# Performance work log

Measured on AMD Instinct MI355X. Metric: run time of the kernel, lower is better.

Reference implementation:

```python
import jax, jax.numpy as jnp
import numpy as np

DIM = 4096
N_HEADS = 32
N_KV = 8
HEAD_DIM = 128
WINDOW = 4096
BSZ = 1
SEQ = 2048
REPEATS = N_HEADS // N_KV
SCALE = HEAD_DIM ** -0.5
NEG_INF = -1e9


def setup_inputs() -> dict:
    key = jax.random.key(0)
    ks = jax.random.split(key, 5)
    x = jax.random.normal(ks[0], (1, BSZ, SEQ, DIM), jnp.float32)
    wq = jax.random.normal(ks[1], (N_HEADS * HEAD_DIM, DIM), jnp.float32) * (DIM ** -0.5)
    wk = jax.random.normal(ks[2], (N_KV * HEAD_DIM, DIM), jnp.float32) * (DIM ** -0.5)
    wv = jax.random.normal(ks[3], (N_KV * HEAD_DIM, DIM), jnp.float32) * (DIM ** -0.5)
    wo = jax.random.normal(ks[4], (DIM, N_HEADS * HEAD_DIM), jnp.float32) * (DIM ** -0.5)
    # rotary frequencies (Mistral/LLaMA style, base 10000)
    inv = 1.0 / (10000.0 ** (np.arange(0, HEAD_DIM, 2, dtype=np.float32) / HEAD_DIM))
    ang = np.outer(np.arange(SEQ, dtype=np.float32), inv)  # [SEQ, HEAD_DIM//2]
    freqs_cos = jnp.asarray(np.cos(ang), jnp.float32)
    freqs_sin = jnp.asarray(np.sin(ang), jnp.float32)
    positions = jnp.arange(SEQ, dtype=jnp.int32)
    # sliding-window causal additive mask [SEQ, SEQ]
    i = np.arange(SEQ)[:, None]
    j = np.arange(SEQ)[None, :]
    allowed = (j <= i) & (j > i - WINDOW)
    mask = jnp.asarray(np.where(allowed, 0.0, NEG_INF).astype(np.float32))
    cache_k = jnp.zeros((BSZ, WINDOW, N_KV, HEAD_DIM), jnp.float32)
    cache_v = jnp.zeros((BSZ, WINDOW, N_KV, HEAD_DIM), jnp.float32)
    return dict(x=x, wq=wq, wk=wk, wv=wv, wo=wo, freqs_cos=freqs_cos,
                freqs_sin=freqs_sin, positions=positions, mask=mask,
                cache_k=cache_k, cache_v=cache_v)


def _rope(x, cos, sin):
    # x: [b, s, h, hd]; pairs (x0,x1),(x2,x3),... treated as complex numbers
    xr = x[..., 0::2]
    xi = x[..., 1::2]
    c = cos[None, :, None, :]
    s = sin[None, :, None, :]
    out_r = xr * c - xi * s
    out_i = xr * s + xi * c
    return jnp.stack([out_r, out_i], axis=-1).reshape(x.shape)


def reference(x, wq, wk, wv, wo, freqs_cos, freqs_sin, positions, mask, cache_k, cache_v):
    b, s = BSZ, SEQ
    xf = x.reshape(b, s, DIM)
    xq = (xf @ wq.T).reshape(b, s, N_HEADS, HEAD_DIM)
    xk = (xf @ wk.T).reshape(b, s, N_KV, HEAD_DIM)
    xv = (xf @ wv.T).reshape(b, s, N_KV, HEAD_DIM)
    xq = _rope(xq, freqs_cos, freqs_sin)
    xk = _rope(xk, freqs_cos, freqs_sin)
    # sliding-window KV cache scatter update (last WINDOW positions, mod WINDOW)
    pos = positions[-WINDOW:] % WINDOW
    cache_k = cache_k.at[:, pos].set(xk[:, -WINDOW:])
    cache_v = cache_v.at[:, pos].set(xv[:, -WINDOW:])
    # prefill branch (positions.shape[0] > 1): attend over current xk/xv
    key = jnp.repeat(xk, REPEATS, axis=2)  # GQA repeat_kv -> [b, s, H, hd]
    val = jnp.repeat(xv, REPEATS, axis=2)
    q = xq.transpose(0, 2, 1, 3)  # [b, H, s, hd]
    k = key.transpose(0, 2, 1, 3)
    v = val.transpose(0, 2, 1, 3)
    scores = jnp.einsum('bhqd,bhkd->bhqk', q, k) * SCALE + mask[None, None]
    probs = jax.nn.softmax(scores, axis=-1)
    out = jnp.einsum('bhqk,bhkd->bhqd', probs, v)
    out = out.transpose(0, 2, 1, 3).reshape(1, b, s, N_HEADS * HEAD_DIM)
    return out @ wo.T, cache_k, cache_v
```

## Files before the change

kernel.cpp:

```cpp
#include <hip/hip_runtime.h>
#include <hip/hip_bf16.h>


typedef __attribute__((ext_vector_type(8))) short short8_t;
typedef __attribute__((ext_vector_type(2))) unsigned uint2_t;
typedef __attribute__((ext_vector_type(8))) __bf16 bf16x8;
typedef __attribute__((ext_vector_type(4))) float f32x4;
typedef __attribute__((ext_vector_type(16))) float f32x16;

#define SEQLEN 2048
#define QSCALE 0.08838834764831845f

__device__ __forceinline__ short f2b(float f) {
  if (!__builtin_isfinite(f)) f = 0.0f;
  union { float f; unsigned u; } v; v.f = f;
  unsigned r = (v.u + 0x7fffu + ((v.u >> 16) & 1u)) >> 16;
  return (short)r;
}
__device__ __forceinline__ float sf(float f) {
  return __builtin_isfinite(f) ? f : 0.0f;
}
__device__ __forceinline__ short8_t cvt8(const float* p) {
  f32x4 a = *(const f32x4*)p;
  f32x4 b = *(const f32x4*)(p + 4);
  short8_t o;
  o[0] = f2b(a[0]); o[1] = f2b(a[1]); o[2] = f2b(a[2]); o[3] = f2b(a[3]);
  o[4] = f2b(b[0]); o[5] = f2b(b[1]); o[6] = f2b(b[2]); o[7] = f2b(b[3]);
  return o;
}
__device__ __forceinline__ unsigned pkb(float lo, float hi) {
  union { float f; unsigned u; } a, b; a.f = lo; b.f = hi;
  unsigned ra = (a.u + 0x7fffu + ((a.u >> 16) & 1u)) >> 16;
  unsigned rb = (b.u + 0x7fffu + ((b.u >> 16) & 1u)) & 0xffff0000u;
  return rb | ra;
}

#define GLD16(gp, lp) __builtin_amdgcn_global_load_lds( \
    (const __attribute__((address_space(1))) void*)(gp), \
    (__attribute__((address_space(3))) void*)(lp), 16, 0, 0)

__global__ __launch_bounds__(256) void cvt_bf16(
    const float* __restrict__ in, short* __restrict__ out)
{
  size_t i = ((size_t)blockIdx.x * 256 + threadIdx.x) * 8;
  *(short8_t*)&out[i] = cvt8(in + i);
}

__global__ __launch_bounds__(256) void gemm_bf(
    const short* __restrict__ A, const short* __restrict__ W,
    float* __restrict__ C1, float* __restrict__ C2,
    int K, int ldc, int splitN)
{
  __shared__ short As[128 * 64];
  __shared__ short Ws[128 * 64];
  const int tid  = threadIdx.x;
  const int lane = tid & 63;
  const int wid  = tid >> 6;
  const int l15  = lane & 15;
  const int l4   = lane >> 4;

  const int nwg = (int)(gridDim.x * gridDim.y);
  int bid = (int)(blockIdx.y * gridDim.x + blockIdx.x);
  int swz = (bid & 7) * (nwg >> 3) + (bid >> 3);
  const int m0 = (swz / (int)gridDim.x) * 128;
  const int n0 = (swz % (int)gridDim.x) * 128;

  const int wr = (wid >> 1) * 64;
  const int wc = (wid & 1) * 64;
  const int srow = tid >> 3;
  const int scol = (tid & 7) * 8;

  f32x4 acc[4][4] = {};

  const short* Ab = A + (size_t)(m0 + srow) * K + scol;
  const short* Wb = W + (size_t)(n0 + srow) * K + scol;

  for (int k0 = 0; k0 < K; k0 += 64) {
#pragma unroll
    for (int i = 0; i < 4; ++i) {
      GLD16(Ab + (size_t)(i * 32) * K + k0, &As[(i * 32 + wid * 8) * 64]);
      GLD16(Wb + (size_t)(i * 32) * K + k0, &Ws[(i * 32 + wid * 8) * 64]);
    }
    __syncthreads();

#pragma unroll
    for (int kk = 0; kk < 2; ++kk) {
      bf16x8 af[4], wf[4];
#pragma unroll
      for (int m = 0; m < 4; ++m)
        af[m] = *(const bf16x8*)&As[(wr + m * 16 + l15) * 64 + kk * 32 + l4 * 8];
#pragma unroll
      for (int n = 0; n < 4; ++n)
        wf[n] = *(const bf16x8*)&Ws[(wc + n * 16 + l15) * 64 + kk * 32 + l4 * 8];
#pragma unroll
      for (int m = 0; m < 4; ++m)
#pragma unroll
        for (int n = 0; n < 4; ++n)
          acc[m][n] = __builtin_amdgcn_mfma_f32_16x16x32_bf16(af[m], wf[n], acc[m][n], 0, 0, 0);
    }
    __syncthreads();
  }

  float* Cb = (n0 < splitN) ? C1 : (C2 - splitN);
#pragma unroll
  for (int m = 0; m < 4; ++m) {
    int rbase = m0 + wr + m * 16 + l4 * 4;
#pragma unroll
    for (int n = 0; n < 4; ++n) {
      int cbase = n0 + wc + n * 16 + l15;
#pragma unroll
      for (int r = 0; r < 4; ++r)
        Cb[(size_t)(rbase + r) * ldc + cbase] = sf(acc[m][n][r]);
    }
  }
}

__device__ __forceinline__ void rope8(const float* in, float* out,
                                      const float* fc, const float* fs, int t, int p0)
{
  f32x4 a = *(const f32x4*)in;
  f32x4 b = *(const f32x4*)(in + 4);
  f32x4 cv = *(const f32x4*)&fc[t * 64 + p0];
  f32x4 sv = *(const f32x4*)&fs[t * 64 + p0];
  float x0[8] = {a[0], a[1], a[2], a[3], b[0], b[1], b[2], b[3]};
#pragma unroll
  for (int i = 0; i < 4; ++i) {
    float xr = x0[2 * i], xi = x0[2 * i + 1];
    out[2 * i]     = sf(xr * cv[i] - xi * sv[i]);
    out[2 * i + 1] = sf(xr * sv[i] + xi * cv[i]);
  }
}

__global__ __launch_bounds__(256) void rope_q_bf(
    const float* __restrict__ q, short* __restrict__ qb,
    const float* __restrict__ fc, const float* __restrict__ fs)
{
  size_t idx = ((size_t)blockIdx.x * 256 + threadIdx.x) * 8;
  int t   = (int)(idx >> 12);
  int col = (int)(idx & 4095);
  float o[8];
  rope8(&q[idx], o, fc, fs, t, (col & 127) >> 1);
  short8_t ob;
#pragma unroll
  for (int i = 0; i < 8; ++i) ob[i] = f2b(o[i] * QSCALE);
  *(short8_t*)&qb[idx] = ob;
}

__global__ __launch_bounds__(256) void rope_k_dual(
    float* __restrict__ ck, short* __restrict__ kb,
    const float* __restrict__ fc, const float* __restrict__ fs)
{
  size_t idx = ((size_t)blockIdx.x * 256 + threadIdx.x) * 8;
  int t   = (int)(idx >> 10);
  int col = (int)(idx & 1023);
  float o[8];
  rope8(&ck[idx], o, fc, fs, t, (col & 127) >> 1);
  *(f32x4*)&ck[idx]     = f32x4{o[0], o[1], o[2], o[3]};
  *(f32x4*)&ck[idx + 4] = f32x4{o[4], o[5], o[6], o[7]};
  short8_t ob;
#pragma unroll
  for (int i = 0; i < 8; ++i) ob[i] = f2b(o[i]);
  *(short8_t*)&kb[idx] = ob;
}

__global__ __launch_bounds__(256) void transpose_v(
    const float* __restrict__ cv, short* __restrict__ Vt)
{
  __shared__ short tile[64][72];
  const int t0 = blockIdx.x * 64;
  const int d0 = blockIdx.y * 64;
  const int h  = blockIdx.z;
  const int tid = threadIdx.x;
  const int r = tid >> 3;
  const int c = (tid & 7) * 8;
#pragma unroll
  for (int it = 0; it < 2; ++it) {
    short8_t v = cvt8(&cv[(size_t)(t0 + it * 32 + r) * 1024 + h * 128 + d0 + c]);
    *(short8_t*)&tile[it * 32 + r][c] = v;
  }
  __syncthreads();
#pragma unroll
  for (int it = 0; it < 2; ++it) {
    int dr = it * 32 + r;
    short8_t v;
#pragma unroll
    for (int i = 0; i < 8; ++i) v[i] = tile[c + i][dr];
    *(short8_t*)&Vt[(size_t)(h * 128 + d0 + dr) * SEQLEN + t0 + c] = v;
  }
}

__global__ __launch_bounds__(128, 2) void attn_fwd4(
    const short* __restrict__ Q,
    const short* __restrict__ Kc,
    const short* __restrict__ Vt,
    short* __restrict__ O)
{
  const int bid = (int)blockIdx.x;
  const int kvh = bid & 7;
  const int j   = bid >> 3;
  const int h   = kvh * 4 + (j & 3);
  const int i   = j >> 2;
  const int qtA = 63 - i, qtB = i;
  const int tid = (int)threadIdx.x;
  const int wid = tid >> 6;
  const int lane = tid & 63;
  const int l31 = lane & 31;
  const int hi  = lane >> 5;

  __shared__ short PA[2][32][88], PB[2][32][88];
  __shared__ float oxch[16][64];
  __shared__ float mlx[2][2][32][2];
  __shared__ float scx[2][2][32];
  __shared__ float rexch[2][64];

  const int q0A = qtA * 32, q0B = qtB * 32;
  const int qgA = q0A + l31, qgB = q0B + l31;
  const int kendA = q0A + 32, kendB = q0B + 32;

  bf16x8 qfA[8], qfB[8];
  {
    const short* qpA = Q + (size_t)qgA * 4096 + h * 128 + hi * 8;
    const short* qpB = Q + (size_t)qgB * 4096 + h * 128 + hi * 8;
#pragma unroll
    for (int ks = 0; ks < 8; ++ks) {
      qfA[ks] = *(const bf16x8*)(qpA + ks * 16);
      qfB[ks] = *(const bf16x8*)(qpB + ks * 16);
    }
  }

  f32x16 oA0 = {}, oA1 = {}, oA2 = {}, oA3 = {};
  f32x16 oB0 = {}, oB1 = {}, oB2 = {}, oB3 = {};
  float mA = -1e30f, lA = 0.f, mB = -1e30f, lB = 0.f;

  for (int kt = wid * 64; kt < kendA; kt += 128) {
    const bool actB = (kt < kendB);
    f32x16 sA0 = {}, sA1 = {}, sB0 = {}, sB1 = {};
    {
      const short* kp = Kc + (size_t)(kt + l31) * 1024 + kvh * 128 + hi * 8;
      __builtin_amdgcn_s_setprio(1);
      if (actB) {
#pragma unroll
        for (int ks = 0; ks < 8; ++ks) {
          bf16x8 k0 = *(const bf16x8*)(kp + ks * 16);
          bf16x8 k1 = *(const bf16x8*)(kp + 32 * 1024 + ks * 16);
          sA0 = __builtin_amdgcn_mfma_f32_32x32x16_bf16(k0, qfA[ks], sA0, 0, 0, 0);
          sA1 = __builtin_amdgcn_mfma_f32_32x32x16_bf16(k1, qfA[ks], sA1, 0, 0, 0);
          sB0 = __builtin_amdgcn_mfma_f32_32x32x16_bf16(k0, qfB[ks], sB0, 0, 0, 0);
          sB1 = __builtin_amdgcn_mfma_f32_32x32x16_bf16(k1, qfB[ks], sB1, 0, 0, 0);
        }
      } else {
#pragma unroll
        for (int ks = 0; ks < 8; ++ks) {
          bf16x8 k0 = *(const bf16x8*)(kp + ks * 16);
          bf16x8 k1 = *(const bf16x8*)(kp + 32 * 1024 + ks * 16);
          sA0 = __builtin_amdgcn_mfma_f32_32x32x16_bf16(k0, qfA[ks], sA0, 0, 0, 0);
          sA1 = __builtin_amdgcn_mfma_f32_32x32x16_bf16(k1, qfA[ks], sA1, 0, 0, 0);
        }
      }
      __builtin_amdgcn_s_setprio(0);
    }

    if (kt + 63 > q0A) {
#pragma unroll
      for (int r = 0; r < 16; ++r) {
        int crow = (r & 3) + 8 * (r >> 2) + 4 * hi;
        if (kt + crow > qgA)      sA0[r] = -1e30f;
        if (kt + 32 + crow > qgA) sA1[r] = -1e30f;
      }
    }
    {
      float t[8];
#pragma unroll
      for (int r = 0; r < 8; ++r)
        t[r] = fmaxf(fmaxf(sA0[r], sA0[r + 8]), fmaxf(sA1[r], sA1[r + 8]));
      float pmax = fmaxf(fmaxf(fmaxf(t[0], t[1]), fmaxf(t[2], t[3])),
                         fmaxf(fmaxf(t[4], t[5]), fmaxf(t[6], t[7])));
      pmax = fmaxf(pmax, __shfl_xor(pmax, 32, 64));
      if (!__all(pmax <= mA + 8.f)) {
        float mnew = fmaxf(mA, pmax);
        float resc = __expf(mA - mnew);
        mA = mnew; lA *= resc;
        if (lane < 32) rexch[wid][l31] = resc;
#pragma unroll
        for (int r = 0; r < 16; ++r) {
          float rs = rexch[wid][(r & 3) + 8 * (r >> 2) + 4 * hi];
          oA0[r] *= rs; oA1[r] *= rs; oA2[r] *= rs; oA3[r] *= rs;
        }
      }
      float psum = 0.f;
#pragma unroll
      for (int r = 0; r < 16; ++r) { sA0[r] = __expf(sA0[r] - mA); psum += sA0[r]; }
#pragma unroll
      for (int r = 0; r < 16; ++r) { sA1[r] = __expf(sA1[r] - mA); psum += sA1[r]; }
      lA += psum + __shfl_xor(psum, 32, 64);
#pragma unroll
      for (int t4 = 0; t4 < 4; ++t4) {
        int c = 8 * t4 + 4 * hi;
        *(uint2_t*)&PA[wid][l31][c]      = uint2_t{pkb(sA0[4*t4], sA0[4*t4+1]), pkb(sA0[4*t4+2], sA0[4*t4+3])};
        *(uint2_t*)&PA[wid][l31][32 + c] = uint2_t{pkb(sA1[4*t4], sA1[4*t4+1]), pkb(sA1[4*t4+2], sA1[4*t4+3])};
      }
    }

    if (actB) {
      if (kt + 63 > q0B) {
#pragma unroll
        for (int r = 0; r < 16; ++r) {
          int crow = (r & 3) + 8 * (r >> 2) + 4 * hi;
          if (kt + crow > qgB)      sB0[r] = -1e30f;
          if (kt + 32 + crow > qgB) sB1[r] = -1e30f;
        }
      }
      float t[8];
#pragma unroll
      for (int r = 0; r < 8; ++r)
        t[r] = fmaxf(fmaxf(sB0[r], sB0[r + 8]), fmaxf(sB1[r], sB1[r + 8]));
      float pmax = fmaxf(fmaxf(fmaxf(t[0], t[1]), fmaxf(t[2], t[3])),
                         fmaxf(fmaxf(t[4], t[5]), fmaxf(t[6], t[7])));
      pmax = fmaxf(pmax, __shfl_xor(pmax, 32, 64));
      if (!__all(pmax <= mB + 8.f)) {
        float mnew = fmaxf(mB, pmax);
        float resc = __expf(mB - mnew);
        mB = mnew; lB *= resc;
        if (lane < 32) rexch[wid][32 + l31] = resc;
#pragma unroll
        for (int r = 0; r < 16; ++r) {
          float rs = rexch[wid][32 + (r & 3) + 8 * (r >> 2) + 4 * hi];
          oB0[r] *= rs; oB1[r] *= rs; oB2[r] *= rs; oB3[r] *= rs;
        }
      }
      float psum = 0.f;
#pragma unroll
      for (int r = 0; r < 16; ++r) { sB0[r] = __expf(sB0[r] - mB); psum += sB0[r]; }
#pragma unroll
      for (int r = 0; r < 16; ++r) { sB1[r] = __expf(sB1[r] - mB); psum += sB1[r]; }
      lB += psum + __shfl_xor(psum, 32, 64);
#pragma unroll
      for (int t4 = 0; t4 < 4; ++t4) {
        int c = 8 * t4 + 4 * hi;
        *(uint2_t*)&PB[wid][l31][c]      = uint2_t{pkb(sB0[4*t4], sB0[4*t4+1]), pkb(sB0[4*t4+2], sB0[4*t4+3])};
        *(uint2_t*)&PB[wid][l31][32 + c] = uint2_t{pkb(sB1[4*t4], sB1[4*t4+1]), pkb(sB1[4*t4+2], sB1[4*t4+3])};
      }
    }

    const short* vb = Vt + (size_t)(kvh * 128 + l31) * SEQLEN + kt + hi * 8;
#pragma unroll
    for (int g = 0; g < 4; ++g) {
      const short* vg = vb + g * 16;
      bf16x8 vf0 = *(const bf16x8*)(vg);
      bf16x8 vf1 = *(const bf16x8*)(vg + 32 * SEQLEN);
      bf16x8 vf2 = *(const bf16x8*)(vg + 64 * SEQLEN);
      bf16x8 vf3 = *(const bf16x8*)(vg + (size_t)96 * SEQLEN);
      bf16x8 pfA = *(const bf16x8*)&PA[wid][l31][g * 16 + hi * 8];
      __builtin_amdgcn_s_setprio(1);
      oA0 = __builtin_amdgcn_mfma_f32_32x32x16_bf16(pfA, vf0, oA0, 0, 0, 0);
      oA1 = __builtin_amdgcn_mfma_f32_32x32x16_bf16(pfA, vf1, oA1, 0, 0, 0);
      oA2 = __builtin_amdgcn_mfma_f32_32x32x16_bf16(pfA, vf2, oA2, 0, 0, 0);
      oA3 = __builtin_amdgcn_mfma_f32_32x32x16_bf16(pfA, vf3, oA3, 0, 0, 0);
      if (actB) {
        bf16x8 pfB = *(const bf16x8*)&PB[wid][l31][g * 16 + hi * 8];
        oB0 = __builtin_amdgcn_mfma_f32_32x32x16_bf16(pfB, vf0, oB0, 0, 0, 0);
        oB1 = __builtin_amdgcn_mfma_f32_32x32x16_bf16(pfB, vf1, oB1, 0, 0, 0);
        oB2 = __builtin_amdgcn_mfma_f32_32x32x16_bf16(pfB, vf2, oB2, 0, 0, 0);
        oB3 = __builtin_amdgcn_mfma_f32_32x32x16_bf16(pfB, vf3, oB3, 0, 0, 0);
      }
      __builtin_amdgcn_s_setprio(0);
    }
  }

  if (lane < 32) {
    mlx[wid][0][l31][0] = mA; mlx[wid][0][l31][1] = lA;
    mlx[wid][1][l31][0] = mB; mlx[wid][1][l31][1] = lB;
  }
  __syncthreads();
  if (wid == 0 && lane < 32) {
#pragma unroll
    for (int T = 0; T < 2; ++T) {
      float m0 = mlx[0][T][l31][0], l0 = mlx[0][T][l31][1];
      float m1 = mlx[1][T][l31][0], l1 = mlx[1][T][l31][1];
      float M  = fmaxf(m0, m1);
      float e0 = __expf(m0 - M), e1 = __expf(m1 - M);
      float den = l0 * e0 + l1 * e1;
      scx[0][T][l31] = e0 / den;
      scx[1][T][l31] = e1 / den;
    }
  }
  __syncthreads();

#define MERGE_STORE(oreg, T, q0, g) do {                                     \
    if (wid == 1) {                                                          \
      _Pragma("unroll")                                                      \
      for (int r = 0; r < 16; ++r)                                           \
        oxch[r][lane] = (oreg)[r] * scx[1][T][(r & 3) + 8 * (r >> 2) + 4 * hi]; \
    }                                                                        \
    __syncthreads();                                                         \
    if (wid == 0) {                                                          \
      _Pragma("unroll")                                                      \
      for (int r = 0; r < 16; ++r) {                                         \
        int crow = (r & 3) + 8 * (r >> 2) + 4 * hi;                          \
        float v = (oreg)[r] * scx[0][T][crow] + oxch[r][lane];               \
        O[(size_t)((q0) + crow) * 4096 + h * 128 + (g) * 32 + l31] = f2b(v); \
      }                                                                      \
    }                                                                        \
    __syncthreads();                                                         \
  } while (0)

  MERGE_STORE(oA0, 0, q0A, 0);
  MERGE_STORE(oA1, 0, q0A, 1);
  MERGE_STORE(oA2, 0, q0A, 2);
  MERGE_STORE(oA3, 0, q0A, 3);
  MERGE_STORE(oB0, 1, q0B, 0);
  MERGE_STORE(oB1, 1, q0B, 1);
  MERGE_STORE(oB2, 1, q0B, 2);
  MERGE_STORE(oB3, 1, q0B, 3);
#undef MERGE_STORE
}

extern "C" void kernel_launch(void* const* d_in, const int* in_sizes, int n_in,
                              void* d_out, int out_size, void* d_ws, size_t ws_size,
                              hipStream_t stream) {
  const float* x  = (const float*)d_in[0];
  const float* wq = (const float*)d_in[1];
  const float* wk = (const float*)d_in[2];
  const float* wv = (const float*)d_in[3];
  const float* wo = (const float*)d_in[4];
  const float* fc = (const float*)d_in[5];
  const float* fs = (const float*)d_in[6];

  float* out = (float*)d_out;
  float* out_main = out;
  float* cache_k  = out + (size_t)2048 * 4096;
  float* cache_v  = cache_k + (size_t)4096 * 8 * 128;

  const size_t MB_W = 33554432;
  const size_t MB_X = 16777216;
  short* slotA = (short*)d_ws;
  short* x_bf  = (short*)((char*)d_ws + MB_W);
  short* attn_out = x_bf;
  short* Vt    = (short*)((char*)d_ws + MB_W + MB_X);
  short* q_bf  = slotA;
  short* k_bf  = slotA + (size_t)2048 * 4096;

  cvt_bf16<<<4096, 256, 0, stream>>>(x, x_bf);
  cvt_bf16<<<8192, 256, 0, stream>>>(wq, slotA);
  gemm_bf<<<dim3(32, 16), 256, 0, stream>>>(x_bf, slotA, out_main, out_main, 4096, 4096, 1 << 30);
  cvt_bf16<<<2048, 256, 0, stream>>>(wk, slotA);
  cvt_bf16<<<2048, 256, 0, stream>>>(wv, slotA + (size_t)1024 * 4096);
  gemm_bf<<<dim3(16, 16), 256, 0, stream>>>(x_bf, slotA, cache_k, cache_v, 4096, 1024, 1024);

  rope_q_bf<<<4096, 256, 0, stream>>>(out_main, q_bf, fc, fs);
  rope_k_dual<<<1024, 256, 0, stream>>>(cache_k, k_bf, fc, fs);
  transpose_v<<<dim3(32, 2, 8), 256, 0, stream>>>(cache_v, Vt);
  hipMemsetAsync(cache_k + (size_t)2048 * 1024, 0, (size_t)2048 * 1024 * 4, stream);
  hipMemsetAsync(cache_v + (size_t)2048 * 1024, 0, (size_t)2048 * 1024 * 4, stream);

  attn_fwd4<<<1024, 128, 0, stream>>>(q_bf, k_bf, Vt, attn_out);

  cvt_bf16<<<8192, 256, 0, stream>>>(wo, slotA);
  gemm_bf<<<dim3(32, 16), 256, 0, stream>>>(attn_out, slotA, out_main, out_main, 4096, 4096, 1 << 30);
}
```

Baseline: 492.8 us.

## Share K/V tiles in LDS across the four GQA heads per block

The attention kernel now launches 256 blocks of 512 threads. Each block serves all four query heads of one KV head, and K and V tiles of 128 keys are staged cooperatively into swizzled LDS. Previously each 2-wave block read K and V straight from global memory for a single head, so the same KV data was fetched four times. The change adds block-wide barriers around each tile load and uses much more shared memory, which limits occupancy. Loads and compute are not double-buffered, so load latency is not overlapped.

Result: slower. 530.6 us (+7.7%).

```diff
diff --git a/kernel.cpp b/kernel.cpp
--- a/kernel.cpp
+++ b/kernel.cpp
@@ -189,7 +189,7 @@
   }
 }
 
-__global__ __launch_bounds__(128, 2) void attn_fwd4(
+__global__ __launch_bounds__(512, 2) void attn_fwd6(
     const short* __restrict__ Q,
     const short* __restrict__ Kc,
     const short* __restrict__ Vt,
@@ -197,21 +197,23 @@
 {
   const int bid = (int)blockIdx.x;
   const int kvh = bid & 7;
-  const int j   = bid >> 3;
-  const int h   = kvh * 4 + (j & 3);
-  const int i   = j >> 2;
+  const int i   = bid >> 3;
   const int qtA = 63 - i, qtB = i;
   const int tid = (int)threadIdx.x;
   const int wid = tid >> 6;
+  const int hs  = wid & 3;
+  const int par = wid >> 2;
+  const int h   = kvh * 4 + hs;
   const int lane = tid & 63;
   const int l31 = lane & 31;
   const int hi  = lane >> 5;
 
-  __shared__ short PA[2][32][88], PB[2][32][88];
-  __shared__ float oxch[16][64];
-  __shared__ float mlx[2][2][32][2];
-  __shared__ float scx[2][2][32];
-  __shared__ float rexch[2][64];
+  __shared__ short Ks[128 * 128];
+  __shared__ short Vs[128 * 128];
+  __shared__ short PA[8][32][72], PB[8][32][72];
+  __shared__ float exch[8][64];
+  __shared__ float mlx[2][4][2][32][2];
+  __shared__ float scx[2][4][2][32];
 
   const int q0A = qtA * 32, q0B = qtB * 32;
   const int qgA = q0A + l31, qgB = q0B + l31;
@@ -232,176 +234,186 @@
   f32x16 oB0 = {}, oB1 = {}, oB2 = {}, oB3 = {};
   float mA = -1e30f, lA = 0.f, mB = -1e30f, lB = 0.f;
 
-  for (int kt = wid * 64; kt < kendA; kt += 128) {
-    const bool actB = (kt < kendB);
-    f32x16 sA0 = {}, sA1 = {}, sB0 = {}, sB1 = {};
-    {
-      const short* kp = Kc + (size_t)(kt + l31) * 1024 + kvh * 128 + hi * 8;
-      __builtin_amdgcn_s_setprio(1);
-      if (actB) {
+  const int xsw = l31 & 15;
+
+  for (int ktb = 0; ktb < kendA; ktb += 128) {
+#pragma unroll
+    for (int it = 0; it < 4; ++it) {
+      int g0  = (wid * 4 + it) * 64;
+      int row = (g0 >> 4) + (lane >> 4);
+      int gch = (lane & 15) ^ (row & 15);
+      GLD16(Kc + (size_t)(ktb + row) * 1024 + kvh * 128 + gch * 8, &Ks[g0 * 8]);
+      GLD16(Vt + (size_t)(kvh * 128 + row) * SEQLEN + ktb + gch * 8, &Vs[g0 * 8]);
+    }
+    __syncthreads();
+
+    const int kt = ktb + par * 64;
+    if (kt < kendA) {
+      const int kb = par * 64;
+      const bool actB = (kt < kendB);
+      f32x16 sA0 = {}, sA1 = {}, sB0 = {}, sB1 = {};
+      {
+        __builtin_amdgcn_s_setprio(1);
 #pragma unroll
         for (int ks = 0; ks < 8; ++ks) {
-          bf16x8 k0 = *(const bf16x8*)(kp + ks * 16);
-          bf16x8 k1 = *(const bf16x8*)(kp + 32 * 1024 + ks * 16);
+          int ch = (ks * 2 + hi) ^ xsw;
+          bf16x8 k0 = *(const bf16x8*)&Ks[(kb + l31) * 128 + ch * 8];
+          bf16x8 k1 = *(const bf16x8*)&Ks[(kb + 32 + l31) * 128 + ch * 8];
           sA0 = __builtin_amdgcn_mfma_f32_32x32x16_bf16(k0, qfA[ks], sA0, 0, 0, 0);
           sA1 = __builtin_amdgcn_mfma_f32_32x32x16_bf16(k1, qfA[ks], sA1, 0, 0, 0);
-          sB0 = __builtin_amdgcn_mfma_f32_32x32x16_bf16(k0, qfB[ks], sB0, 0, 0, 0);
-          sB1 = __builtin_amdgcn_mfma_f32_32x32x16_bf16(k1, qfB[ks], sB1, 0, 0, 0);
-        }
-      } else {
-#pragma unroll
-        for (int ks = 0; ks < 8; ++ks) {
-          bf16x8 k0 = *(const bf16x8*)(kp + ks * 16);
-          bf16x8 k1 = *(const bf16x8*)(kp + 32 * 1024 + ks * 16);
-          sA0 = __builtin_amdgcn_mfma_f32_32x32x16_bf16(k0, qfA[ks], sA0, 0, 0, 0);
-          sA1 = __builtin_amdgcn_mfma_f32_32x32x16_bf16(k1, qfA[ks], sA1, 0, 0, 0);
-        }
+          if (actB) {
+            sB0 = __builtin_amdgcn_mfma_f32_32x32x16_bf16(k0, qfB[ks], sB0, 0, 0, 0);
+            sB1 = __builtin_amdgcn_mfma_f32_32x32x16_bf16(k1, qfB[ks], sB1, 0, 0, 0);
+          }
+        }
+        __builtin_amdgcn_s_setprio(0);
       }
-      __builtin_amdgcn_s_setprio(0);
-    }
-
-    if (kt + 63 > q0A) {
-#pragma unroll
-      for (int r = 0; r < 16; ++r) {
-        int crow = (r & 3) + 8 * (r >> 2) + 4 * hi;
-        if (kt + crow > qgA)      sA0[r] = -1e30f;
-        if (kt + 32 + crow > qgA) sA1[r] = -1e30f;
-      }
-    }
-    {
-      float t[8];
-#pragma unroll
-      for (int r = 0; r < 8; ++r)
-        t[r] = fmaxf(fmaxf(sA0[r], sA0[r + 8]), fmaxf(sA1[r], sA1[r + 8]));
-      float pmax = fmaxf(fmaxf(fmaxf(t[0], t[1]), fmaxf(t[2], t[3])),
-                         fmaxf(fmaxf(t[4], t[5]), fmaxf(t[6], t[7])));
-      pmax = fmaxf(pmax, __shfl_xor(pmax, 32, 64));
-      if (!__all(pmax <= mA + 8.f)) {
-        float mnew = fmaxf(mA, pmax);
-        float resc = __expf(mA - mnew);
-        mA = mnew; lA *= resc;
-        if (lane < 32) rexch[wid][l31] = resc;
-#pragma unroll
-        for (int r = 0; r < 16; ++r) {
-          float rs = rexch[wid][(r & 3) + 8 * (r >> 2) + 4 * hi];
-          oA0[r] *= rs; oA1[r] *= rs; oA2[r] *= rs; oA3[r] *= rs;
-        }
-      }
-      float psum = 0.f;
-#pragma unroll
-      for (int r = 0; r < 16; ++r) { sA0[r] = __expf(sA0[r] - mA); psum += sA0[r]; }
-#pragma unroll
-      for (int r = 0; r < 16; ++r) { sA1[r] = __expf(sA1[r] - mA); psum += sA1[r]; }
-      lA += psum + __shfl_xor(psum, 32, 64);
-#pragma unroll
-      for (int t4 = 0; t4 < 4; ++t4) {
-        int c = 8 * t4 + 4 * hi;
-        *(uint2_t*)&PA[wid][l31][c]      = uint2_t{pkb(sA0[4*t4], sA0[4*t4+1]), pkb(sA0[4*t4+2], sA0[4*t4+3])};
-        *(uint2_t*)&PA[wid][l31][32 + c] = uint2_t{pkb(sA1[4*t4], sA1[4*t4+1]), pkb(sA1[4*t4+2], sA1[4*t4+3])};
-      }
-    }
-
-    if (actB) {
-      if (kt + 63 > q0B) {
+
+      if (kt + 63 > q0A) {
 #pragma unroll
         for (int r = 0; r < 16; ++r) {
           int crow = (r & 3) + 8 * (r >> 2) + 4 * hi;
-          if (kt + crow > qgB)      sB0[r] = -1e30f;
-          if (kt + 32 + crow > qgB) sB1[r] = -1e30f;
+          if (kt + crow > qgA)      sA0[r] = -1e30f;
+          if (kt + 32 + crow > qgA) sA1[r] = -1e30f;
         }
       }
-      float t[8];
-#pragma unroll
-      for (int r = 0; r < 8; ++r)
-        t[r] = fmaxf(fmaxf(sB0[r], sB0[r + 8]), fmaxf(sB1[r], sB1[r + 8]));
-      float pmax = fmaxf(fmaxf(fmaxf(t[0], t[1]), fmaxf(t[2], t[3])),
-                         fmaxf(fmaxf(t[4], t[5]), fmaxf(t[6], t[7])));
-      pmax = fmaxf(pmax, __shfl_xor(pmax, 32, 64));
-      if (!__all(pmax <= mB + 8.f)) {
-        float mnew = fmaxf(mB, pmax);
-        float resc = __expf(mB - mnew);
-        mB = mnew; lB *= resc;
-        if (lane < 32) rexch[wid][32 + l31] = resc;
-#pragma unroll
-        for (int r = 0; r < 16; ++r) {
-          float rs = rexch[wid][32 + (r & 3) + 8 * (r >> 2) + 4 * hi];
-          oB0[r] *= rs; oB1[r] *= rs; oB2[r] *= rs; oB3[r] *= rs;
+      {
+        float t[8];
+#pragma unroll
+        for (int r = 0; r < 8; ++r)
+          t[r] = fmaxf(fmaxf(sA0[r], sA0[r + 8]), fmaxf(sA1[r], sA1[r + 8]));
+        float pmax = fmaxf(fmaxf(fmaxf(t[0], t[1]), fmaxf(t[2], t[3])),
+                           fmaxf(fmaxf(t[4], t[5]), fmaxf(t[6], t[7])));
+        pmax = fmaxf(pmax, __shfl_xor(pmax, 32, 64));
+        if (!__all(pmax <= mA + 8.f)) {
+          float mnew = fmaxf(mA, pmax);
+          float resc = __expf(mA - mnew);
+          mA = mnew; lA *= resc;
+          if (lane < 32) exch[wid][l31] = resc;
+#pragma unroll
+          for (int r = 0; r < 16; ++r) {
+            float rs = exch[wid][(r & 3) + 8 * (r >> 2) + 4 * hi];
+            oA0[r] *= rs; oA1[r] *= rs; oA2[r] *= rs; oA3[r] *= rs;
+          }
+        }
+        float psum = 0.f;
+#pragma unroll
+        for (int r = 0; r < 16; ++r) { sA0[r] = __expf(sA0[r] - mA); psum += sA0[r]; }
+#pragma unroll
+        for (int r = 0; r < 16; ++r) { sA1[r] = __expf(sA1[r] - mA); psum += sA1[r]; }
+        lA += psum + __shfl_xor(psum, 32, 64);
+#pragma unroll
+        for (int t4 = 0; t4 < 4; ++t4) {
+          int c = 8 * t4 + 4 * hi;
+          *(uint2_t*)&PA[wid][l31][c]      = uint2_t{pkb(sA0[4*t4], sA0[4*t4+1]), pkb(sA0[4*t4+2], sA0[4*t4+3])};
+          *(uint2_t*)&PA[wid][l31][32 + c] = uint2_t{pkb(sA1[4*t4], sA1[4*t4+1]), pkb(sA1[4*t4+2], sA1[4*t4+3])};
         }
       }
-      float psum = 0.f;
-#pragma unroll
-      for (int r = 0; r < 16; ++r) { sB0[r] = __expf(sB0[r] - mB); psum += sB0[r]; }
-#pragma unroll
-      for (int r = 0; r < 16; ++r) { sB1[r] = __expf(sB1[r] - mB); psum += sB1[r]; }
-      lB += psum + __shfl_xor(psum, 32, 64);
-#pragma unroll
-      for (int t4 = 0; t4 < 4; ++t4) {
-        int c = 8 * t4 + 4 * hi;
-        *(uint2_t*)&PB[wid][l31][c]      = uint2_t{pkb(sB0[4*t4], sB0[4*t4+1]), pkb(sB0[4*t4+2], sB0[4*t4+3])};
-        *(uint2_t*)&PB[wid][l31][32 + c] = uint2_t{pkb(sB1[4*t4], sB1[4*t4+1]), pkb(sB1[4*t4+2], sB1[4*t4+3])};
+
+      if (actB) {
+        if (kt + 63 > q0B) {
+#pragma unroll
+          for (int r = 0; r < 16; ++r) {
+            int crow = (r & 3) + 8 * (r >> 2) + 4 * hi;
+            if (kt + crow > qgB)      sB0[r] = -1e30f;
+            if (kt + 32 + crow > qgB) sB1[r] = -1e30f;
+          }
+        }
+        float t[8];
+#pragma unroll
+        for (int r = 0; r < 8; ++r)
+          t[r] = fmaxf(fmaxf(sB0[r], sB0[r + 8]), fmaxf(sB1[r], sB1[r + 8]));
+        float pmax = fmaxf(fmaxf(fmaxf(t[0], t[1]), fmaxf(t[2], t[3])),
+                           fmaxf(fmaxf(t[4], t[5]), fmaxf(t[6], t[7])));
+        pmax = fmaxf(pmax, __shfl_xor(pmax, 32, 64));
+        if (!__all(pmax <= mB + 8.f)) {
+          float mnew = fmaxf(mB, pmax);
+          float resc = __expf(mB - mnew);
+          mB = mnew; lB *= resc;
+          if (lane < 32) exch[wid][32 + l31] = resc;
+#pragma unroll
+          for (int r = 0; r < 16; ++r) {
+            float rs = exch[wid][32 + (r & 3) + 8 * (r >> 2) + 4 * hi];
+            oB0[r] *= rs; oB1[r] *= rs; oB2[r] *= rs; oB3[r] *= rs;
+          }
+        }
+        float psum = 0.f;
+#pragma unroll
+        for (int r = 0; r < 16; ++r) { sB0[r] = __expf(sB0[r] - mB); psum += sB0[r]; }
+#pragma unroll
+        for (int r = 0; r < 16; ++r) { sB1[r] = __expf(sB1[r] - mB); psum += sB1[r]; }
+        lB += psum + __shfl_xor(psum, 32, 64);
+#pragma unroll
+        for (int t4 = 0; t4 < 4; ++t4) {
+          int c = 8 * t4 + 4 * hi;
+          *(uint2_t*)&PB[wid][l31][c]      = uint2_t{pkb(sB0[4*t4], sB0[4*t4+1]), pkb(sB0[4*t4+2], sB0[4*t4+3])};
+          *(uint2_t*)&PB[wid][l31][32 + c] = uint2_t{pkb(sB1[4*t4], sB1[4*t4+1]), pkb(sB1[4*t4+2], sB1[4*t4+3])};
+        }
       }
-    }
-
-    const short* vb = Vt + (size_t)(kvh * 128 + l31) * SEQLEN + kt + hi * 8;
-#pragma unroll
-    for (int g = 0; g < 4; ++g) {
-      const short* vg = vb + g * 16;
-      bf16x8 vf0 = *(const bf16x8*)(vg);
-      bf16x8 vf1 = *(const bf16x8*)(vg + 32 * SEQLEN);
-      bf16x8 vf2 = *(const bf16x8*)(vg + 64 * SEQLEN);
-      bf16x8 vf3 = *(const bf16x8*)(vg + (size_t)96 * SEQLEN);
-      bf16x8 pfA = *(const bf16x8*)&PA[wid][l31][g * 16 + hi * 8];
-      __builtin_amdgcn_s_setprio(1);
-      oA0 = __builtin_amdgcn_mfma_f32_32x32x16_bf16(pfA, vf0, oA0, 0, 0, 0);
-      oA1 = __builtin_amdgcn_mfma_f32_32x32x16_bf16(pfA, vf1, oA1, 0, 0, 0);
-      oA2 = __builtin_amdgcn_mfma_f32_32x32x16_bf16(pfA, vf2, oA2, 0, 0, 0);
-      oA3 = __builtin_amdgcn_mfma_f32_32x32x16_bf16(pfA, vf3, oA3, 0, 0, 0);
-      if (actB) {
-        bf16x8 pfB = *(const bf16x8*)&PB[wid][l31][g * 16 + hi * 8];
-        oB0 = __builtin_amdgcn_mfma_f32_32x32x16_bf16(pfB, vf0, oB0, 0, 0, 0);
-        oB1 = __builtin_amdgcn_mfma_f32_32x32x16_bf16(pfB, vf1, oB1, 0, 0, 0);
-        oB2 = __builtin_amdgcn_mfma_f32_32x32x16_bf16(pfB, vf2, oB2, 0, 0, 0);
-        oB3 = __builtin_amdgcn_mfma_f32_32x32x16_bf16(pfB, vf3, oB3, 0, 0, 0);
+
+#pragma unroll
+      for (int g = 0; g < 4; ++g) {
+        int chl = par * 8 + g * 2 + hi;
+        bf16x8 vf0 = *(const bf16x8*)&Vs[(l31)      * 128 + (chl ^ xsw) * 8];
+        bf16x8 vf1 = *(const bf16x8*)&Vs[(32 + l31) * 128 + (chl ^ xsw) * 8];
+        bf16x8 vf2 = *(const bf16x8*)&Vs[(64 + l31) * 128 + (chl ^ xsw) * 8];
+        bf16x8 vf3 = *(const bf16x8*)&Vs[(96 + l31) * 128 + (chl ^ xsw) * 8];
+        bf16x8 pfA = *(const bf16x8*)&PA[wid][l31][g * 16 + hi * 8];
+        __builtin_amdgcn_s_setprio(1);
+        oA0 = __builtin_amdgcn_mfma_f32_32x32x16_bf16(pfA, vf0, oA0, 0, 0, 0);
+        oA1 = __builtin_amdgcn_mfma_f32_32x32x16_bf16(pfA, vf1, oA1, 0, 0, 0);
+        oA2 = __builtin_amdgcn_mfma_f32_32x32x16_bf16(pfA, vf2, oA2, 0, 0, 0);
+        oA3 = __builtin_amdgcn_mfma_f32_32x32x16_bf16(pfA, vf3, oA3, 0, 0, 0);
+        if (actB) {
+          bf16x8 pfB = *(const bf16x8*)&PB[wid][l31][g * 16 + hi * 8];
+          oB0 = __builtin_amdgcn_mfma_f32_32x32x16_bf16(pfB, vf0, oB0, 0, 0, 0);
+          oB1 = __builtin_amdgcn_mfma_f32_32x32x16_bf16(pfB, vf1, oB1, 0, 0, 0);
+          oB2 = __builtin_amdgcn_mfma_f32_32x32x16_bf16(pfB, vf2, oB2, 0, 0, 0);
+          oB3 = __builtin_amdgcn_mfma_f32_32x32x16_bf16(pfB, vf3, oB3, 0, 0, 0);
+        }
+        __builtin_amdgcn_s_setprio(0);
       }
-      __builtin_amdgcn_s_setprio(0);
-    }
+    }
+    __syncthreads();
   }
 
   if (lane < 32) {
-    mlx[wid][0][l31][0] = mA; mlx[wid][0][l31][1] = lA;
-    mlx[wid][1][l31][0] = mB; mlx[wid][1][l31][1] = lB;
+    mlx[par][hs][0][l31][0] = mA; mlx[par][hs][0][l31][1] = lA;
+    mlx[par][hs][1][l31][0] = mB; mlx[par][hs][1][l31][1] = lB;
   }
   __syncthreads();
-  if (wid == 0 && lane < 32) {
+  if (par == 0 && lane < 32) {
 #pragma unroll
     for (int T = 0; T < 2; ++T) {
-      float m0 = mlx[0][T][l31][0], l0 = mlx[0][T][l31][1];
-      float m1 = mlx[1][T][l31][0], l1 = mlx[1][T][l31][1];
+      float m0 = mlx[0][hs][T][l31][0], l0 = mlx[0][hs][T][l31][1];
+      float m1 = mlx[1][hs][T][l31][0], l1 = mlx[1][hs][T][l31][1];
       float M  = fmaxf(m0, m1);
       float e0 = __expf(m0 - M), e1 = __expf(m1 - M);
       float den = l0 * e0 + l1 * e1;
-      scx[0][T][l31] = e0 / den;
-      scx[1][T][l31] = e1 / den;
+      scx[0][hs][T][l31] = e0 / den;
+      scx[1][hs][T][l31] = e1 / den;
     }
   }
   __syncthreads();
 
-#define MERGE_STORE(oreg, T, q0, g) do {                                     \
-    if (wid == 1) {                                                          \
-      _Pragma("unroll")                                                      \
-      for (int r = 0; r < 16; ++r)                                           \
-        oxch[r][lane] = (oreg)[r] * scx[1][T][(r & 3) + 8 * (r >> 2) + 4 * hi]; \
-    }                                                                        \
-    __syncthreads();                                                         \
-    if (wid == 0) {                                                          \
-      _Pragma("unroll")                                                      \
-      for (int r = 0; r < 16; ++r) {                                         \
-        int crow = (r & 3) + 8 * (r >> 2) + 4 * hi;                          \
-        float v = (oreg)[r] * scx[0][T][crow] + oxch[r][lane];               \
-        O[(size_t)((q0) + crow) * 4096 + h * 128 + (g) * 32 + l31] = f2b(v); \
-      }                                                                      \
-    }                                                                        \
-    __syncthreads();                                                         \
+  float* ox = (float*)(&PA[0][0][0]) + hs * 1024;
+
+#define MERGE_STORE(oreg, T, q0, g) do {                                       \
+    if (par == 1) {                                                            \
+      _Pragma("unroll")                                                        \
+      for (int r = 0; r < 16; ++r)                                             \
+        ox[r * 64 + lane] = (oreg)[r] * scx[1][hs][T][(r & 3) + 8 * (r >> 2) + 4 * hi]; \
+    }                                                                          \
+    __syncthreads();                                                           \
+    if (par == 0) {                                                            \
+      _Pragma("unroll")                                                        \
+      for (int r = 0; r < 16; ++r) {                                           \
+        int crow = (r & 3) + 8 * (r >> 2) + 4 * hi;                            \
+        float v = (oreg)[r] * scx[0][hs][T][crow] + ox[r * 64 + lane];         \
+        O[(size_t)((q0) + crow) * 4096 + h * 128 + (g) * 32 + l31] = f2b(v);   \
+      }                                                                        \
+    }                                                                          \
+    __syncthreads();                                                           \
   } while (0)
 
   MERGE_STORE(oA0, 0, q0A, 0);
@@ -453,7 +465,7 @@
   hipMemsetAsync(cache_k + (size_t)2048 * 1024, 0, (size_t)2048 * 1024 * 4, stream);
   hipMemsetAsync(cache_v + (size_t)2048 * 1024, 0, (size_t)2048 * 1024 * 4, stream);
 
-  attn_fwd4<<<1024, 128, 0, stream>>>(q_bf, k_bf, Vt, attn_out);
+  attn_fwd6<<<256, 512, 0, stream>>>(q_bf, k_bf, Vt, attn_out);
 
   cvt_bf16<<<8192, 256, 0, stream>>>(wo, slotA);
   gemm_bf<<<dim3(32, 16), 256, 0, stream>>>(attn_out, slotA, out_main, out_main, 4096, 4096, 1 << 30);
```
